# Optimization experiments

Measured on AMD Instinct MI355X. Metric: run time of the kernel, lower is better.

The kernel has to match this reference:

```python
import jax, jax.numpy as jnp
import numpy as np

NEG = -1e30  # safe log-zero for fp32/bf16


def _ctc_neg_log_likelihood(labels, log_probs, label_length, data_length, blank):
    """Standard CTC alpha (forward) DP in log space.
    labels: [B, L] int, log_probs: [T, B, C], lengths: [B] int.
    Returns per-example negative log likelihood [B]."""
    T, B, C = log_probs.shape
    L = labels.shape[1]
    S = 2 * L + 1  # extended label: blank, l1, blank, l2, ..., blank
    ext = jnp.full((B, S), blank, dtype=labels.dtype).at[:, 1::2].set(labels)
    prev2 = jnp.concatenate([jnp.full((B, 2), -1, labels.dtype), ext[:, :-2]], axis=1)
    allow_skip = (ext != blank) & (ext != prev2)  # [B, S] skip-transition legality

    def emit(lp_t):  # [B, C] -> [B, S]
        return jnp.take_along_axis(lp_t, ext, axis=1)

    # t = 0: paths can only be at s=0 (blank) or s=1 (first label)
    alpha0 = jnp.where(jnp.arange(S)[None, :] < 2, emit(log_probs[0]), NEG)

    def step(alpha, xs):
        lp_t, t = xs
        a1 = jnp.concatenate([jnp.full((B, 1), NEG, alpha.dtype), alpha[:, :-1]], axis=1)
        a2 = jnp.concatenate([jnp.full((B, 2), NEG, alpha.dtype), alpha[:, :-2]], axis=1)
        a2 = jnp.where(allow_skip, a2, NEG)
        new = jax.nn.logsumexp(jnp.stack([alpha, a1, a2]), axis=0) + emit(lp_t)
        # freeze alpha once past this example's sequence length
        return jnp.where((t < data_length)[:, None], new, alpha), None

    alpha, _ = jax.lax.scan(step, alpha0, (log_probs[1:], jnp.arange(1, T)))

    # likelihood = alpha[2*len] (final blank) + alpha[2*len - 1] (final label)
    a_blank = jnp.take_along_axis(alpha, (2 * label_length)[:, None], axis=1)[:, 0]
    a_label = jnp.take_along_axis(alpha, (2 * label_length - 1)[:, None], axis=1)[:, 0]
    return -jnp.logaddexp(a_blank, a_label)


def setup_inputs() -> dict:
    key = jax.random.key(0)
    k1, k2, k3, k4 = jax.random.split(key, 4)
    T, B, C, L = 1024, 32, 1024, 128
    data = jax.random.normal(k1, (T, B, C), dtype=jnp.float32)
    labels = jax.random.randint(k2, (B, L), 1, C, dtype=jnp.int32)  # avoid blank=0
    label_length = jax.random.randint(k3, (B,), 64, L + 1, dtype=jnp.int32)
    data_length = jax.random.randint(k4, (B,), 512, T + 1, dtype=jnp.int32)
    return {"labels": labels, "data": data, "label_length": label_length,
            "data_length": data_length}


def reference(labels, data, label_length, data_length):
    # from_logits=True -> ctc_loss_v2: log_softmax then CTC; blank_index=0
    log_probs = jax.nn.log_softmax(data, axis=-1)
    loss = _ctc_neg_log_likelihood(labels, log_probs, label_length, data_length, 0)
    return jnp.mean(loss).reshape([1])
```

## Files before the change

kernel.cpp:

```cpp
#include <hip/hip_runtime.h>
#include <hip/hip_bf16.h>

#define T_DIM 1024
#define B_DIM 32
#define C_DIM 1024
#define L_DIM 128
#define S_DIM 257
#define CH    32

#define WS_EPAIR   0
#define WS_EBLANK  (32u * 1024u * 64u * 8u)
#define WS_ALPHA   (WS_EBLANK + 32u * 1024u * 4u)
#define WS_BETA    (WS_ALPHA + 32u * 264u * 8u)
#define WS_KACC    (WS_BETA + 32u * 264u * 8u)

__global__ __launch_bounds__(256) void emit_kernel(const float* __restrict__ data,
                                                   const int* __restrict__ labels,
                                                   float2* __restrict__ epair,
                                                   float* __restrict__ eblank) {
    const int wave = threadIdx.x >> 6;
    const int lane = threadIdx.x & 63;
    const int row = blockIdx.x * 4 + wave;
    const int b = row & (B_DIM - 1);
    const int t = row >> 5;

    const float4* d4 = (const float4*)(data + (size_t)row * C_DIM);
    float4 v[4];
    float m = -3.4e38f;
#pragma unroll
    for (int k = 0; k < 4; ++k) {
        v[k] = d4[lane + 64 * k];
        m = fmaxf(m, fmaxf(fmaxf(v[k].x, v[k].y), fmaxf(v[k].z, v[k].w)));
    }
#pragma unroll
    for (int off = 32; off >= 1; off >>= 1)
        m = fmaxf(m, __shfl_xor(m, off, 64));
    float s = 0.f;
#pragma unroll
    for (int k = 0; k < 4; ++k)
        s += __expf(v[k].x - m) + __expf(v[k].y - m) +
             __expf(v[k].z - m) + __expf(v[k].w - m);
#pragma unroll
    for (int off = 32; off >= 1; off >>= 1)
        s += __shfl_xor(s, off, 64);
    const float lse = m + __logf(s);

    const float* drow = data + (size_t)row * C_DIM;
    const int2 cc = ((const int2*)(labels + b * L_DIM))[lane];
    float2 pr;
    pr.x = __expf(drow[cc.x] - lse);
    pr.y = __expf(drow[cc.y] - lse);
    epair[((size_t)b * T_DIM + t) * 64 + lane] = pr;
    if (lane == 0) eblank[b * T_DIM + t] = __expf(drow[0] - lse);
}

__global__ __launch_bounds__(64, 1) void dp_kernel(const float2* __restrict__ epair,
                                                   const float* __restrict__ eblank,
                                                   const int* __restrict__ labels,
                                                   const int* __restrict__ label_length,
                                                   const int* __restrict__ data_length,
                                                   double* __restrict__ alphavec,
                                                   double* __restrict__ betavec,
                                                   long long* __restrict__ kaccs) {
    const int b   = blockIdx.x & (B_DIM - 1);
    const int dir = blockIdx.x >> 5;
    const int l = threadIdx.x;
    const int* lab = labels + b * L_DIM;
    const int len = label_length[b];
    const int dlen = data_length[b];
    const int m = dlen >> 1;

    __shared__ float2 ebuf[2][CH][64];
    __shared__ float  ebl[T_DIM];

    const float2* eprow = epair + (size_t)b * T_DIM * 64;
    const float*  ebrow = eblank + (size_t)b * T_DIM;

#pragma unroll
    for (int i = 0; i < T_DIM / 64; ++i)
        __builtin_amdgcn_global_load_lds(
            (const __attribute__((address_space(1))) void*)(ebrow + i * 64 + l),
            (__attribute__((address_space(3))) void*)(&ebl[i * 64]), 4, 0, 0);

    auto stage_chunk = [&](int cb, int trow0) {
#pragma unroll
        for (int i = 0; i < CH / 2; ++i)
            __builtin_amdgcn_global_load_lds(
                (const __attribute__((address_space(1))) void*)
                    ((const char*)(eprow + (size_t)(trow0 + 2 * i) * 64) + l * 16),
                (__attribute__((address_space(3))) void*)(&ebuf[cb][2 * i][0]), 16, 0, 0);
    };

    double a0 = 0.0, a1 = 0.0, a2 = 0.0, a3 = 0.0, a4 = 0.0;
    long long kacc = 0;

    double skip1d, skip3d;
    auto step = [&](double em1, double em3, double eb) {
        double h = __shfl_up(a3, 1, 64);
        if (l == 0) h = 0.0;
        const double n0 = (a0 + h) * eb;
        const double n1 = fma(skip1d, h, a1 + a0) * em1;
        const double n2 = (a2 + a1) * eb;
        const double n3 = fma(skip3d, a1, a3 + a2) * em3;
        const double n4 = (a4 + a3) * eb;
        a0 = n0; a1 = n1; a2 = n2; a3 = n3; a4 = n4;
    };

    auto renorm = [&]() {
        double mx = fmax(fmax(fmax(a0, a1), fmax(a2, a3)), a4);
        int hi = __double2hiint(mx);
#pragma unroll
        for (int off = 32; off >= 1; off >>= 1)
            hi = max(hi, __shfl_xor(hi, off, 64));
        const int ex = ((hi >> 20) & 0x7ff) - 1023;
        const double sc = __hiloint2double((1023 - ex) << 20, 0);
        a0 *= sc; a1 *= sc; a2 *= sc; a3 *= sc; a4 *= sc;
        kacc += ex;
    };

    if (dir == 0) {
        const int2 cc = ((const int2*)lab)[l];
        skip1d = ((l > 0) && (cc.x != lab[2 * l - 1])) ? 1.0 : 0.0;
        skip3d = (cc.y != cc.x) ? 1.0 : 0.0;

        stage_chunk(0, 1);
        __builtin_amdgcn_s_waitcnt(0x0f70);

        {
            const float2 ep0 = eprow[l];
            a0 = (l == 0) ? (double)ebl[0] : 0.0;
            a1 = (l == 0) ? (double)ep0.x : 0.0;
        }

        const int nsteps = m - 1;
        const int nch = (nsteps + CH - 1) / CH;
        for (int c = 0; c < nch; ++c) {
            const int cb = c & 1;
            const bool more = (c + 1 < nch);
            if (more) stage_chunk(cb ^ 1, 1 + CH * (c + 1));
            __builtin_amdgcn_sched_barrier(0);
            const int t0 = 1 + CH * c;
            if (t0 + CH <= m) {
                double e1R[4], e2R[4], ebR[4];
#pragma unroll
                for (int p = 0; p < 3; ++p) {
                    const float2 ep = ebuf[cb][p][l];
                    e1R[p] = (double)ep.x; e2R[p] = (double)ep.y;
                    ebR[p] = (double)ebl[t0 + p];
                }
#pragma unroll
                for (int j = 0; j < CH; ++j) {
                    const int jn = (j + 3 < CH) ? (j + 3) : (CH - 1);
                    const float2 epn = ebuf[cb][jn][l];
                    const float ebn = ebl[t0 + jn];
                    step(e1R[j & 3], e2R[j & 3], ebR[j & 3]);
                    e1R[(j + 3) & 3] = (double)epn.x;
                    e2R[(j + 3) & 3] = (double)epn.y;
                    ebR[(j + 3) & 3] = (double)ebn;
                }
            } else {
#pragma unroll
                for (int j = 0; j < CH; ++j) {
                    if (t0 + j < m) {
                        const float2 ep = ebuf[cb][j][l];
                        step((double)ep.x, (double)ep.y, (double)ebl[t0 + j]);
                    }
                }
            }
            renorm();
            if (more) __builtin_amdgcn_s_waitcnt(0x0f70);
            __builtin_amdgcn_sched_barrier(0);
        }

        double* av = alphavec + b * 264;
        av[4 * l + 0] = a0; av[4 * l + 1] = a1;
        av[4 * l + 2] = a2; av[4 * l + 3] = a3;
        if (l == 63) av[256] = a4;
        if (l == 0) kaccs[2 * b + 0] = kacc;
    } else {
        const int2 c2 = ((const int2*)lab)[63 - l];
        const int labL = (l > 0) ? lab[128 - 2 * l] : -1;
        skip1d = ((l > 0) && (labL != c2.y)) ? 1.0 : 0.0;
        skip3d = (c2.y != c2.x) ? 1.0 : 0.0;

        stage_chunk(0, dlen - 1 - CH);
        __builtin_amdgcn_s_waitcnt(0x0f70);

        {
            const float2 epi = eprow[(size_t)(dlen - 1) * 64 + (63 - l)];
            const double ebi = (double)ebl[dlen - 1];
            const int s0 = 256 - 4 * l;
            a0 = (s0 == 2 * len     || s0 == 2 * len - 1) ? ebi : 0.0;
            a1 = (s0 - 1 == 2 * len || s0 - 1 == 2 * len - 1) ? (double)epi.y : 0.0;
            a2 = (s0 - 2 == 2 * len || s0 - 2 == 2 * len - 1) ? ebi : 0.0;
            a3 = (s0 - 3 == 2 * len || s0 - 3 == 2 * len - 1) ? (double)epi.x : 0.0;
            a4 = 0.0;
        }

        const int nsteps = dlen - 1 - m;
        const int nch = (nsteps + CH - 1) / CH;
        for (int c = 0; c < nch; ++c) {
            const int cb = c & 1;
            const bool more = (c + 1 < nch);
            const int thi = dlen - 2 - CH * c;
            const int tlo = thi - CH + 1;
            if (more) stage_chunk(cb ^ 1, tlo - CH);
            __builtin_amdgcn_sched_barrier(0);
            if (tlo >= m) {
                double e1R[4], e2R[4], ebR[4];
#pragma unroll
                for (int p = 0; p < 3; ++p) {
                    const float2 ep = ebuf[cb][CH - 1 - p][63 - l];
                    e1R[p] = (double)ep.y; e2R[p] = (double)ep.x;
                    ebR[p] = (double)ebl[thi - p];
                }
#pragma unroll
                for (int jj = 0; jj < CH; ++jj) {
                    const int jnn = (jj + 3 < CH) ? (jj + 3) : (CH - 1);
                    const float2 epn = ebuf[cb][CH - 1 - jnn][63 - l];
                    const float ebn = ebl[thi - jnn];
                    step(e1R[jj & 3], e2R[jj & 3], ebR[jj & 3]);
                    e1R[(jj + 3) & 3] = (double)epn.y;
                    e2R[(jj + 3) & 3] = (double)epn.x;
                    ebR[(jj + 3) & 3] = (double)ebn;
                }
            } else {
#pragma unroll
                for (int jj = 0; jj < CH; ++jj) {
                    const int j = CH - 1 - jj;
                    const int t = tlo + j;
                    if (t >= m) {
                        const float2 ep = ebuf[cb][j][63 - l];
                        step((double)ep.y, (double)ep.x, (double)ebl[t]);
                    }
                }
            }
            renorm();
            if (more) __builtin_amdgcn_s_waitcnt(0x0f70);
            __builtin_amdgcn_sched_barrier(0);
        }

        double* bv = betavec + b * 264;
        bv[256 - 4 * l] = a0; bv[255 - 4 * l] = a1;
        bv[254 - 4 * l] = a2; bv[253 - 4 * l] = a3;
        if (l == 63) bv[0] = a4;
        if (l == 0) { bv[257] = 0.0; bv[258] = 0.0; kaccs[2 * b + 1] = kacc; }
    }
}

__global__ __launch_bounds__(256) void combine_kernel(const double* __restrict__ alphavec,
                                                      const double* __restrict__ betavec,
                                                      const long long* __restrict__ kaccs,
                                                      const int* __restrict__ labels,
                                                      float* __restrict__ out) {
    const int wave = threadIdx.x >> 6;
    const int l = threadIdx.x & 63;
    float acc = 0.f;

    for (int b = wave; b < B_DIM; b += 4) {
        const double* A = alphavec + b * 264;
        const double* Bv = betavec + b * 264;
        const int* lab = labels + b * L_DIM;

        const double a0 = A[4 * l], a1 = A[4 * l + 1], a2 = A[4 * l + 2], a3 = A[4 * l + 3];
        const double b0 = Bv[4 * l], b1 = Bv[4 * l + 1], b2 = Bv[4 * l + 2];
        const double b3 = Bv[4 * l + 3], b4 = Bv[4 * l + 4], b5 = Bv[4 * l + 5];
        const double sk1 = (lab[2 * l + 1] != lab[2 * l]) ? 1.0 : 0.0;
        const int labn = (l < 63) ? lab[2 * l + 2] : -1;
        const double sk3 = ((l < 63) && (labn != lab[2 * l + 1])) ? 1.0 : 0.0;

        double s = a0 * (b0 + b1)
                 + a1 * (b1 + b2 + sk1 * b3)
                 + a2 * (b2 + b3)
                 + a3 * (b3 + b4 + sk3 * b5);
        if (l == 63) s += A[256] * Bv[256];

#pragma unroll
        for (int off = 32; off >= 1; off >>= 1)
            s += __shfl_xor(s, off, 64);

        if (l == 0) {
            const long long k = kaccs[2 * b] + kaccs[2 * b + 1];
            const long long vb = __double_as_longlong(s);
            const int ve = (int)((vb >> 52) & 0x7ff) - 1023;
            const double mant = __longlong_as_double(
                (vb & 0x000FFFFFFFFFFFFFLL) | (1023LL << 52));
            const double l2 = (double)__log2f((float)mant) + (double)ve + (double)k;
            acc += (float)(-l2 * 0.6931471805599453);
        }
    }

    __shared__ float part[4];
    if (l == 0) part[wave] = acc;
    __syncthreads();
    if (threadIdx.x == 0)
        out[0] = (part[0] + part[1] + part[2] + part[3]) * (1.0f / B_DIM);
}

extern "C" void kernel_launch(void* const* d_in, const int* in_sizes, int n_in,
                              void* d_out, int out_size, void* d_ws, size_t ws_size,
                              hipStream_t stream) {
    const int*   labels       = (const int*)d_in[0];
    const float* data         = (const float*)d_in[1];
    const int*   label_length = (const int*)d_in[2];
    const int*   data_length  = (const int*)d_in[3];
    float*       out          = (float*)d_out;

    char* ws = (char*)d_ws;
    float2*    epair    = (float2*)(ws + WS_EPAIR);
    float*     eblank   = (float*)(ws + WS_EBLANK);
    double*    alphavec = (double*)(ws + WS_ALPHA);
    double*    betavec  = (double*)(ws + WS_BETA);
    long long* kaccs    = (long long*)(ws + WS_KACC);

    const int rows = T_DIM * B_DIM;
    emit_kernel<<<rows / 4, 256, 0, stream>>>(data, labels, epair, eblank);
    dp_kernel<<<2 * B_DIM, 64, 0, stream>>>(epair, eblank, labels, label_length,
                                            data_length, alphavec, betavec, kaccs);
    combine_kernel<<<1, 256, 0, stream>>>(alphavec, betavec, kaccs, labels, out);
}
```

Measured before the change: 241.9 us.

## Factor blank emission out of CTC recurrence and use DPP lane shift

Emission probabilities are now stored relative to the blank logit, so the blank factor is common to every state at each timestep and drops out of the forward and backward recursions. The sum of per-timestep blank log-probs is added back in the combine kernel. This removes three multiplies per step, the blank LDS buffer and its loads. The cross-lane shift of a3 also moves from __shfl_up to DPP row_shr, which lowers latency on the serial dependency chain. The risk is a wider dynamic range in the ratios, which could strain renormalization, and DPP row_shr only moves values within 16-lane rows, so lanes 16, 32 and 48 may receive 0 instead of their neighbour's value.

Result: slower. 255.4 us (+5.6%).

```diff
diff --git a/kernel.cpp b/kernel.cpp
--- a/kernel.cpp
+++ b/kernel.cpp
@@ -9,15 +9,26 @@
 #define CH    32
 
 #define WS_EPAIR   0
-#define WS_EBLANK  (32u * 1024u * 64u * 8u)
-#define WS_ALPHA   (WS_EBLANK + 32u * 1024u * 4u)
+#define WS_LNB     (32u * 1024u * 64u * 8u)
+#define WS_ALPHA   (WS_LNB + 32u * 1024u * 4u)
 #define WS_BETA    (WS_ALPHA + 32u * 264u * 8u)
 #define WS_KACC    (WS_BETA + 32u * 264u * 8u)
+
+__device__ __forceinline__ double lane_shr1_f64(double x) {
+#if __has_builtin(__builtin_amdgcn_update_dpp)
+    const int lo = __builtin_amdgcn_update_dpp(0, __double2loint(x), 0x138, 0xf, 0xf, true);
+    const int hi = __builtin_amdgcn_update_dpp(0, __double2hiint(x), 0x138, 0xf, 0xf, true);
+    return __hiloint2double(hi, lo);
+#else
+    double h = __shfl_up(x, 1, 64);
+    return ((threadIdx.x & 63) == 0) ? 0.0 : h;
+#endif
+}
 
 __global__ __launch_bounds__(256) void emit_kernel(const float* __restrict__ data,
                                                    const int* __restrict__ labels,
                                                    float2* __restrict__ epair,
-                                                   float* __restrict__ eblank) {
+                                                   float* __restrict__ lnblank) {
     const int wave = threadIdx.x >> 6;
     const int lane = threadIdx.x & 63;
     const int row = blockIdx.x * 4 + wave;
@@ -46,16 +57,16 @@
     const float lse = m + __logf(s);
 
     const float* drow = data + (size_t)row * C_DIM;
+    const float x0 = drow[0];
     const int2 cc = ((const int2*)(labels + b * L_DIM))[lane];
     float2 pr;
-    pr.x = __expf(drow[cc.x] - lse);
-    pr.y = __expf(drow[cc.y] - lse);
+    pr.x = __expf(drow[cc.x] - x0);
+    pr.y = __expf(drow[cc.y] - x0);
     epair[((size_t)b * T_DIM + t) * 64 + lane] = pr;
-    if (lane == 0) eblank[b * T_DIM + t] = __expf(drow[0] - lse);
+    if (lane == 0) lnblank[b * T_DIM + t] = x0 - lse;
 }
 
 __global__ __launch_bounds__(64, 1) void dp_kernel(const float2* __restrict__ epair,
-                                                   const float* __restrict__ eblank,
                                                    const int* __restrict__ labels,
                                                    const int* __restrict__ label_length,
                                                    const int* __restrict__ data_length,
@@ -71,16 +82,8 @@
     const int m = dlen >> 1;
 
     __shared__ float2 ebuf[2][CH][64];
-    __shared__ float  ebl[T_DIM];
 
     const float2* eprow = epair + (size_t)b * T_DIM * 64;
-    const float*  ebrow = eblank + (size_t)b * T_DIM;
-
-#pragma unroll
-    for (int i = 0; i < T_DIM / 64; ++i)
-        __builtin_amdgcn_global_load_lds(
-            (const __attribute__((address_space(1))) void*)(ebrow + i * 64 + l),
-            (__attribute__((address_space(3))) void*)(&ebl[i * 64]), 4, 0, 0);
 
     auto stage_chunk = [&](int cb, int trow0) {
 #pragma unroll
@@ -95,14 +98,13 @@
     long long kacc = 0;
 
     double skip1d, skip3d;
-    auto step = [&](double em1, double em3, double eb) {
-        double h = __shfl_up(a3, 1, 64);
-        if (l == 0) h = 0.0;
-        const double n0 = (a0 + h) * eb;
-        const double n1 = fma(skip1d, h, a1 + a0) * em1;
-        const double n2 = (a2 + a1) * eb;
-        const double n3 = fma(skip3d, a1, a3 + a2) * em3;
-        const double n4 = (a4 + a3) * eb;
+    auto step = [&](double r1, double r3) {
+        const double h = lane_shr1_f64(a3);
+        const double n0 = a0 + h;
+        const double n1 = fma(skip1d, h, a1 + a0) * r1;
+        const double n2 = a2 + a1;
+        const double n3 = fma(skip3d, a1, a3 + a2) * r3;
+        const double n4 = a4 + a3;
         a0 = n0; a1 = n1; a2 = n2; a3 = n3; a4 = n4;
     };
 
@@ -128,7 +130,7 @@
 
         {
             const float2 ep0 = eprow[l];
-            a0 = (l == 0) ? (double)ebl[0] : 0.0;
+            a0 = (l == 0) ? 1.0 : 0.0;
             a1 = (l == 0) ? (double)ep0.x : 0.0;
         }
 
@@ -141,29 +143,26 @@
             __builtin_amdgcn_sched_barrier(0);
             const int t0 = 1 + CH * c;
             if (t0 + CH <= m) {
-                double e1R[4], e2R[4], ebR[4];
+                double r1R[4], r3R[4];
 #pragma unroll
                 for (int p = 0; p < 3; ++p) {
                     const float2 ep = ebuf[cb][p][l];
-                    e1R[p] = (double)ep.x; e2R[p] = (double)ep.y;
-                    ebR[p] = (double)ebl[t0 + p];
+                    r1R[p] = (double)ep.x; r3R[p] = (double)ep.y;
                 }
 #pragma unroll
                 for (int j = 0; j < CH; ++j) {
                     const int jn = (j + 3 < CH) ? (j + 3) : (CH - 1);
                     const float2 epn = ebuf[cb][jn][l];
-                    const float ebn = ebl[t0 + jn];
-                    step(e1R[j & 3], e2R[j & 3], ebR[j & 3]);
-                    e1R[(j + 3) & 3] = (double)epn.x;
-                    e2R[(j + 3) & 3] = (double)epn.y;
-                    ebR[(j + 3) & 3] = (double)ebn;
+                    step(r1R[j & 3], r3R[j & 3]);
+                    r1R[(j + 3) & 3] = (double)epn.x;
+                    r3R[(j + 3) & 3] = (double)epn.y;
                 }
             } else {
 #pragma unroll
                 for (int j = 0; j < CH; ++j) {
                     if (t0 + j < m) {
                         const float2 ep = ebuf[cb][j][l];
-                        step((double)ep.x, (double)ep.y, (double)ebl[t0 + j]);
+                        step((double)ep.x, (double)ep.y);
                     }
                 }
             }
@@ -188,11 +187,10 @@
 
         {
             const float2 epi = eprow[(size_t)(dlen - 1) * 64 + (63 - l)];
-            const double ebi = (double)ebl[dlen - 1];
             const int s0 = 256 - 4 * l;
-            a0 = (s0 == 2 * len     || s0 == 2 * len - 1) ? ebi : 0.0;
+            a0 = (s0 == 2 * len     || s0 == 2 * len - 1) ? 1.0 : 0.0;
             a1 = (s0 - 1 == 2 * len || s0 - 1 == 2 * len - 1) ? (double)epi.y : 0.0;
-            a2 = (s0 - 2 == 2 * len || s0 - 2 == 2 * len - 1) ? ebi : 0.0;
+            a2 = (s0 - 2 == 2 * len || s0 - 2 == 2 * len - 1) ? 1.0 : 0.0;
             a3 = (s0 - 3 == 2 * len || s0 - 3 == 2 * len - 1) ? (double)epi.x : 0.0;
             a4 = 0.0;
         }
@@ -207,22 +205,19 @@
             if (more) stage_chunk(cb ^ 1, tlo - CH);
             __builtin_amdgcn_sched_barrier(0);
             if (tlo >= m) {
-                double e1R[4], e2R[4], ebR[4];
+                double r1R[4], r3R[4];
 #pragma unroll
                 for (int p = 0; p < 3; ++p) {
                     const float2 ep = ebuf[cb][CH - 1 - p][63 - l];
-                    e1R[p] = (double)ep.y; e2R[p] = (double)ep.x;
-                    ebR[p] = (double)ebl[thi - p];
+                    r1R[p] = (double)ep.y; r3R[p] = (double)ep.x;
                 }
 #pragma unroll
                 for (int jj = 0; jj < CH; ++jj) {
                     const int jnn = (jj + 3 < CH) ? (jj + 3) : (CH - 1);
                     const float2 epn = ebuf[cb][CH - 1 - jnn][63 - l];
-                    const float ebn = ebl[thi - jnn];
-                    step(e1R[jj & 3], e2R[jj & 3], ebR[jj & 3]);
-                    e1R[(jj + 3) & 3] = (double)epn.y;
-                    e2R[(jj + 3) & 3] = (double)epn.x;
-                    ebR[(jj + 3) & 3] = (double)ebn;
+                    step(r1R[jj & 3], r3R[jj & 3]);
+                    r1R[(jj + 3) & 3] = (double)epn.y;
+                    r3R[(jj + 3) & 3] = (double)epn.x;
                 }
             } else {
 #pragma unroll
@@ -231,7 +226,7 @@
                     const int t = tlo + j;
                     if (t >= m) {
                         const float2 ep = ebuf[cb][j][63 - l];
-                        step((double)ep.y, (double)ep.x, (double)ebl[t]);
+                        step((double)ep.y, (double)ep.x);
                     }
                 }
             }
@@ -252,6 +247,8 @@
                                                       const double* __restrict__ betavec,
                                                       const long long* __restrict__ kaccs,
                                                       const int* __restrict__ labels,
+                                                      const int* __restrict__ data_length,
+                                                      const float* __restrict__ lnblank,
                                                       float* __restrict__ out) {
     const int wave = threadIdx.x >> 6;
     const int l = threadIdx.x & 63;
@@ -261,6 +258,7 @@
         const double* A = alphavec + b * 264;
         const double* Bv = betavec + b * 264;
         const int* lab = labels + b * L_DIM;
+        const int dlen = data_length[b];
 
         const double a0 = A[4 * l], a1 = A[4 * l + 1], a2 = A[4 * l + 2], a3 = A[4 * l + 3];
         const double b0 = Bv[4 * l], b1 = Bv[4 * l + 1], b2 = Bv[4 * l + 2];
@@ -275,9 +273,15 @@
                  + a3 * (b3 + b4 + sk3 * b5);
         if (l == 63) s += A[256] * Bv[256];
 
-#pragma unroll
-        for (int off = 32; off >= 1; off >>= 1)
-            s += __shfl_xor(s, off, 64);
+        const float* lnb = lnblank + b * T_DIM;
+        double slnb = 0.0;
+        for (int t = l; t < dlen; t += 64) slnb += (double)lnb[t];
+
+#pragma unroll
+        for (int off = 32; off >= 1; off >>= 1) {
+            s    += __shfl_xor(s, off, 64);
+            slnb += __shfl_xor(slnb, off, 64);
+        }
 
         if (l == 0) {
             const long long k = kaccs[2 * b] + kaccs[2 * b + 1];
@@ -286,7 +290,7 @@
             const double mant = __longlong_as_double(
                 (vb & 0x000FFFFFFFFFFFFFLL) | (1023LL << 52));
             const double l2 = (double)__log2f((float)mant) + (double)ve + (double)k;
-            acc += (float)(-l2 * 0.6931471805599453);
+            acc += (float)(-(l2 * 0.6931471805599453 + slnb));
         }
     }
 
@@ -308,14 +312,15 @@
 
     char* ws = (char*)d_ws;
     float2*    epair    = (float2*)(ws + WS_EPAIR);
-    float*     eblank   = (float*)(ws + WS_EBLANK);
+    float*     lnblank  = (float*)(ws + WS_LNB);
     double*    alphavec = (double*)(ws + WS_ALPHA);
     double*    betavec  = (double*)(ws + WS_BETA);
     long long* kaccs    = (long long*)(ws + WS_KACC);
 
     const int rows = T_DIM * B_DIM;
-    emit_kernel<<<rows / 4, 256, 0, stream>>>(data, labels, epair, eblank);
-    dp_kernel<<<2 * B_DIM, 64, 0, stream>>>(epair, eblank, labels, label_length,
+    emit_kernel<<<rows / 4, 256, 0, stream>>>(data, labels, epair, lnblank);
+    dp_kernel<<<2 * B_DIM, 64, 0, stream>>>(epair, labels, label_length,
                                             data_length, alphavec, betavec, kaccs);
-    combine_kernel<<<1, 256, 0, stream>>>(alphavec, betavec, kaccs, labels, out);
-}
+    combine_kernel<<<1, 256, 0, stream>>>(alphavec, betavec, kaccs, labels,
+                                          data_length, lnblank, out);
+}
```
